# Kernel optimization log

Measured on AMD Instinct MI355X. Metric: run time of the kernel, lower is better.

## Reference

```python
import jax, jax.numpy as jnp
import numpy as np

N_NODES = 100000
N_EDGES = 1600000
F_IN = 128      # dataset.num_features
HID = 128       # hidden_dim (heads=1)
HID_POST = 128  # hidden_dim_post
EDGE_DIM = 16
N_CLASSES = 16
NEG_SLOPE = 0.2  # PyG GATConv default leaky_relu slope


def setup_inputs() -> dict:
    key = jax.random.key(0)
    ks = jax.random.split(key, 16)
    s = 0.1  # weight scale
    inp = {
        "x": jax.random.normal(ks[0], (N_NODES, F_IN), jnp.float32),
        "edge_attr": jax.random.normal(ks[1], (N_EDGES, EDGE_DIM), jnp.float32),
        "W0": jax.random.normal(ks[2], (F_IN, HID), jnp.float32) * s,
        "a_src0": jax.random.normal(ks[3], (HID,), jnp.float32) * s,
        "a_dst0": jax.random.normal(ks[4], (HID,), jnp.float32) * s,
        "We0": jax.random.normal(ks[5], (EDGE_DIM, HID), jnp.float32) * s,
        "a_e0": jax.random.normal(ks[6], (HID,), jnp.float32) * s,
        "b0": jnp.zeros((HID,), jnp.float32),
        "W1": jax.random.normal(ks[7], (HID, HID), jnp.float32) * s,
        "a_src1": jax.random.normal(ks[8], (HID,), jnp.float32) * s,
        "a_dst1": jax.random.normal(ks[9], (HID,), jnp.float32) * s,
        "We1": jax.random.normal(ks[10], (EDGE_DIM, HID), jnp.float32) * s,
        "a_e1": jax.random.normal(ks[11], (HID,), jnp.float32) * s,
        "b1": jnp.zeros((HID,), jnp.float32),
        "lin1_w": jax.random.normal(ks[12], (HID, HID_POST), jnp.float32) * s,
        "lin1_b": jnp.zeros((HID_POST,), jnp.float32),
        "lin2_w": jax.random.normal(ks[13], (HID_POST, N_CLASSES), jnp.float32) * s,
        "lin2_b": jnp.zeros((N_CLASSES,), jnp.float32),
        "edge_index": jax.random.randint(ks[14], (2, N_EDGES), 0, N_NODES, jnp.int64),
    }
    return inp


def gat_conv(x, src, dst, edge_attr, W, a_s, a_d, We, a_e, b):
    """PyG GATConv, heads=1, edge_dim set, add_self_loops=True (fill_value='mean')."""
    n = x.shape[0]
    xl = x @ W                       # [N, HID] shared lin for src/dst
    alpha_src_n = xl @ a_s           # [N]
    alpha_dst_n = xl @ a_d           # [N]
    # self loops: edge_attr filled with per-target-node mean of incoming edge_attr
    deg = jax.ops.segment_sum(jnp.ones(src.shape[0], x.dtype), dst, num_segments=n)
    ea_mean = jax.ops.segment_sum(edge_attr, dst, num_segments=n) / jnp.maximum(deg, 1.0)[:, None]
    loop = jnp.arange(n, dtype=src.dtype)
    src_f = jnp.concatenate([src, loop])
    dst_f = jnp.concatenate([dst, loop])
    ea_f = jnp.concatenate([edge_attr, ea_mean], axis=0)  # [E+N, EDGE_DIM]
    alpha_edge = (ea_f @ We) @ a_e                        # [E+N]
    alpha = jax.nn.leaky_relu(
        alpha_src_n[src_f] + alpha_dst_n[dst_f] + alpha_edge, NEG_SLOPE
    )
    # segment softmax over destination node (every node has its self loop -> nonempty)
    amax = jax.ops.segment_max(alpha, dst_f, num_segments=n)
    ex = jnp.exp(alpha - amax[dst_f])
    denom = jax.ops.segment_sum(ex, dst_f, num_segments=n)
    w = ex / denom[dst_f]                                 # [E+N]
    out = jax.ops.segment_sum(xl[src_f] * w[:, None], dst_f, num_segments=n)
    return out + b


def reference(x, edge_attr, W0, a_src0, a_dst0, We0, a_e0, b0,
              W1, a_src1, a_dst1, We1, a_e1, b1,
              lin1_w, lin1_b, lin2_w, lin2_b, edge_index):
    src, dst = edge_index[0], edge_index[1]
    # dropout layers are identity in eval mode
    h = jax.nn.relu(gat_conv(x, src, dst, edge_attr, W0, a_src0, a_dst0, We0, a_e0, b0))
    h = jax.nn.relu(gat_conv(h, src, dst, edge_attr, W1, a_src1, a_dst1, We1, a_e1, b1))
    h = jax.nn.relu(h @ lin1_w + lin1_b)
    logits = h @ lin2_w + lin2_b
    return jax.nn.log_softmax(logits, axis=-1)
```

## Files before the change

kernel.cpp:

```cpp
#include <hip/hip_runtime.h>
#include <math.h>

#define N_NODES 100000
#define N_EDGES 1600000
#define NEG 0.2f
#define MAXDEG 128
#define WPB 4

__device__ __forceinline__ float lrelu(float x){ return x > 0.f ? x : NEG*x; }
__device__ __forceinline__ unsigned short f2bf(float f){
  unsigned int u = __float_as_uint(f);
  u += 0x7FFFu + ((u >> 16) & 1u);
  return (unsigned short)(u >> 16);
}

__global__ __launch_bounds__(256) void k_deg(const int* __restrict__ dst, int* __restrict__ deg){
  int e = blockIdx.x*256 + threadIdx.x;
  if (e < N_EDGES) atomicAdd(&deg[dst[e]], 1);
}

__global__ __launch_bounds__(256) void k_scan_a(const int* __restrict__ deg, int* __restrict__ incl, int* __restrict__ bsum){
  __shared__ int s[256];
  int t = threadIdx.x; int i = blockIdx.x*256 + t;
  int v = (i < N_NODES) ? deg[i] : 0;
  s[t] = v; __syncthreads();
  for (int off=1; off<256; off<<=1){
    int u = (t>=off)? s[t-off] : 0; __syncthreads();
    s[t] += u; __syncthreads();
  }
  if (i < N_NODES) incl[i] = s[t];
  if (t == 255) bsum[blockIdx.x] = s[t];
}
__global__ __launch_bounds__(512) void k_scan_b(const int* __restrict__ bsum, int* __restrict__ bexcl, int nb,
    const float* __restrict__ We0, const float* __restrict__ ae0,
    const float* __restrict__ We1, const float* __restrict__ ae1, float* __restrict__ wea01){
  __shared__ int s[512];
  int t = threadIdx.x;
  int v = (t<nb)? bsum[t] : 0;
  s[t] = v; __syncthreads();
  for (int off=1; off<512; off<<=1){
    int u = (t>=off)? s[t-off] : 0; __syncthreads();
    s[t] += u; __syncthreads();
  }
  if (t<nb) bexcl[t] = s[t]-v;
  if (t < 16){
    float acc = 0.f;
    for (int j=0;j<128;j++) acc += We0[t*128+j]*ae0[j];
    wea01[t]=acc;
  } else if (t < 32){
    int r = t - 16;
    float acc = 0.f;
    for (int j=0;j<128;j++) acc += We1[r*128+j]*ae1[j];
    wea01[t]=acc;
  }
}
__global__ __launch_bounds__(256) void k_scan_c(const int* __restrict__ incl, const int* __restrict__ deg,
    const int* __restrict__ bexcl, int* __restrict__ rowptr){
  int i = blockIdx.x*256+threadIdx.x;
  if (i < N_NODES) rowptr[i] = incl[i] - deg[i] + bexcl[blockIdx.x];
  if (i == 0) rowptr[N_NODES] = N_EDGES;
}

__global__ __launch_bounds__(256) void k_fillf(const int* __restrict__ src, const int* __restrict__ dst,
     const int* __restrict__ rowptr, int* __restrict__ fill,
     const float* __restrict__ eatt, const float* __restrict__ wea01, uint4* __restrict__ csr){
  int e = blockIdx.x*256+threadIdx.x;
  if (e >= N_EDGES) return;
  const float4* w4 = (const float4*)wea01;
  float4 u0=w4[0], u1=w4[1], u2=w4[2], u3=w4[3];
  float4 v0=w4[4], v1=w4[5], v2=w4[6], v3=w4[7];
  const float4* p = (const float4*)(eatt + (size_t)e*16);
  float4 a0=p[0], a1=p[1], a2=p[2], a3=p[3];
  float ae0 = a0.x*u0.x+a0.y*u0.y+a0.z*u0.z+a0.w*u0.w
            + a1.x*u1.x+a1.y*u1.y+a1.z*u1.z+a1.w*u1.w
            + a2.x*u2.x+a2.y*u2.y+a2.z*u2.z+a2.w*u2.w
            + a3.x*u3.x+a3.y*u3.y+a3.z*u3.z+a3.w*u3.w;
  float ae1 = a0.x*v0.x+a0.y*v0.y+a0.z*v0.z+a0.w*v0.w
            + a1.x*v1.x+a1.y*v1.y+a1.z*v1.z+a1.w*v1.w
            + a2.x*v2.x+a2.y*v2.y+a2.z*v2.z+a2.w*v2.w
            + a3.x*v3.x+a3.y*v3.y+a3.z*v3.z+a3.w*v3.w;
  int d = dst[e];
  int pos = rowptr[d] + atomicAdd(&fill[d], 1);
  csr[pos] = make_uint4((unsigned)src[e], __float_as_uint(ae0), __float_as_uint(ae1), 0u);
}

__global__ __launch_bounds__(256) void k_gemm(const float* __restrict__ X, const float* __restrict__ W,
    const float* __restrict__ bias, float* __restrict__ Y, unsigned short* __restrict__ Ybf,
    const float* __restrict__ a_s, const float* __restrict__ a_d,
    float* __restrict__ asrc, float* __restrict__ adst, int M, int relu){
  __shared__ float Xs[16][68];
  __shared__ float Ws[16][128];
  __shared__ float as_s[128], ad_s[128];
  int t = threadIdx.x;
  if (a_s && t < 128){ as_s[t] = a_s[t]; ad_s[t] = a_d[t]; }
  int row0 = blockIdx.x * 64;
  int tc = t & 15, tr = t >> 4;
  int c0 = tc*8, r0 = tr*4;
  int lr = t >> 2, lc = (t & 3) << 2;
  int wk = t >> 4, wc = (t & 15) * 8;
  float acc[4][8];
  #pragma unroll
  for (int i=0;i<4;i++)
    #pragma unroll
    for (int j=0;j<8;j++) acc[i][j]=0.f;
  int gr = row0 + lr;
  for (int k0=0; k0<128; k0+=16){
    float4 xv = make_float4(0.f,0.f,0.f,0.f);
    if (gr < M) xv = *(const float4*)(X + (size_t)gr*128 + k0 + lc);
    float4 wv0 = *(const float4*)(W + (size_t)(k0+wk)*128 + wc);
    float4 wv1 = *(const float4*)(W + (size_t)(k0+wk)*128 + wc + 4);
    __syncthreads();
    Xs[lc+0][lr]=xv.x; Xs[lc+1][lr]=xv.y; Xs[lc+2][lr]=xv.z; Xs[lc+3][lr]=xv.w;
    *(float4*)&Ws[wk][wc]   = wv0;
    *(float4*)&Ws[wk][wc+4] = wv1;
    __syncthreads();
    #pragma unroll
    for (int kk=0;kk<16;kk++){
      float4 a  = *(const float4*)&Xs[kk][r0];
      float4 b0 = *(const float4*)&Ws[kk][c0];
      float4 b1 = *(const float4*)&Ws[kk][c0+4];
      float av[4] = {a.x,a.y,a.z,a.w};
      float bv[8] = {b0.x,b0.y,b0.z,b0.w,b1.x,b1.y,b1.z,b1.w};
      #pragma unroll
      for (int i=0;i<4;i++)
        #pragma unroll
        for (int j=0;j<8;j++) acc[i][j] += av[i]*bv[j];
    }
  }
  #pragma unroll
  for (int i=0;i<4;i++){
    int r = row0 + r0 + i;
    float v[8];
    #pragma unroll
    for (int j=0;j<8;j++){
      float u = acc[i][j] + (bias ? bias[c0+j] : 0.f);
      v[j] = relu ? fmaxf(u, 0.f) : u;
    }
    if (r < M){
      if (Y){
        *(float4*)(Y + (size_t)r*128 + c0)     = make_float4(v[0],v[1],v[2],v[3]);
        *(float4*)(Y + (size_t)r*128 + c0 + 4) = make_float4(v[4],v[5],v[6],v[7]);
      }
      if (Ybf){
        uint4 pk;
        pk.x = (unsigned)f2bf(v[0]) | ((unsigned)f2bf(v[1])<<16);
        pk.y = (unsigned)f2bf(v[2]) | ((unsigned)f2bf(v[3])<<16);
        pk.z = (unsigned)f2bf(v[4]) | ((unsigned)f2bf(v[5])<<16);
        pk.w = (unsigned)f2bf(v[6]) | ((unsigned)f2bf(v[7])<<16);
        *(uint4*)(Ybf + (size_t)r*128 + c0) = pk;
      }
    }
    if (a_s){
      float s=0.f, d=0.f;
      #pragma unroll
      for (int j=0;j<8;j++){ s += v[j]*as_s[c0+j]; d += v[j]*ad_s[c0+j]; }
      #pragma unroll
      for (int off=1; off<16; off<<=1){ s += __shfl_xor(s,off); d += __shfl_xor(d,off); }
      if ((t & 15)==0 && r < M){ asrc[r]=s; adst[r]=d; }
    }
  }
}

__global__ __launch_bounds__(256) void k_agg(const int* __restrict__ rowptr, const uint4* __restrict__ csr,
    const float* __restrict__ asrc, const float* __restrict__ adst,
    const unsigned short* __restrict__ xlbf,
    const float* __restrict__ bias, float* __restrict__ out, int relu, int layer){
  int w = threadIdx.x >> 6;
  int lane = threadIdx.x & 63;
  int n = blockIdx.x * WPB + w;
  __shared__ float wbuf[WPB][MAXDEG];
  __shared__ int   sbuf[WPB][MAXDEG];
  const unsigned int* xb = (const unsigned int*)xlbf;
  int s0 = rowptr[n], s1 = rowptr[n+1];
  int deg = s1 - s0;
  float adst_n = adst[n];
  float m_edge = -1e30f;
  float sae = 0.f;
  for (int base=0; base<deg; base+=64){
    int i = base + lane;
    float a = -1e30f;
    if (i < deg){
      uint4 p4 = csr[s0 + i];
      int sx = (int)p4.x;
      float ae = __uint_as_float(layer ? p4.z : p4.y);
      float av = lrelu(asrc[sx] + adst_n + ae);
      if (i < MAXDEG){ wbuf[w][i] = av; sbuf[w][i] = sx; }
      a = av;
      sae += ae;
    }
    for (int off=32; off; off>>=1) a = fmaxf(a, __shfl_xor(a, off));
    m_edge = fmaxf(m_edge, a);
  }
  for (int off=32; off; off>>=1) sae += __shfl_xor(sae, off);
  float aloop_n = sae / fmaxf((float)deg, 1.f);
  float al = lrelu(asrc[n] + adst_n + aloop_n);
  float m = fmaxf(m_edge, al);
  float p = 0.f;
  for (int i=lane; i<deg; i+=64){
    float av;
    if (i < MAXDEG) av = wbuf[w][i];
    else { uint4 p4 = csr[s0+i];
           av = lrelu(asrc[p4.x] + adst_n + __uint_as_float(layer ? p4.z : p4.y)); }
    float ev = __expf(av - m);
    if (i < MAXDEG) wbuf[w][i] = ev;
    p += ev;
  }
  for (int off=32; off; off>>=1) p += __shfl_xor(p, off);
  float wl = __expf(al - m);
  float denom = p + wl;
  __syncthreads();
  int g = lane >> 4, cl = lane & 15;
  float acc[8];
  #pragma unroll
  for (int j=0;j<8;j++) acc[j]=0.f;
  if (g == 0){
    uint4 v = *(const uint4*)(xb + (size_t)n*64 + cl*4);
    unsigned int uu[4] = {v.x,v.y,v.z,v.w};
    #pragma unroll
    for (int q=0;q<4;q++){
      acc[2*q]   += wl * __uint_as_float(uu[q] << 16);
      acc[2*q+1] += wl * __uint_as_float(uu[q] & 0xFFFF0000u);
    }
  }
  for (int i=0; i<deg; i+=4){
    int idx = i + g;
    int sx = n; float we = 0.f;
    if (idx < deg){
      if (idx < MAXDEG){ sx = sbuf[w][idx]; we = wbuf[w][idx]; }
      else {
        uint4 p4 = csr[s0+idx]; sx = (int)p4.x;
        we = __expf(lrelu(asrc[sx] + adst_n + __uint_as_float(layer ? p4.z : p4.y)) - m);
      }
    }
    uint4 v = *(const uint4*)(xb + (size_t)sx*64 + cl*4);
    unsigned int uu[4] = {v.x,v.y,v.z,v.w};
    #pragma unroll
    for (int q=0;q<4;q++){
      acc[2*q]   += we * __uint_as_float(uu[q] << 16);
      acc[2*q+1] += we * __uint_as_float(uu[q] & 0xFFFF0000u);
    }
  }
  #pragma unroll
  for (int j=0;j<8;j++){
    acc[j] += __shfl_xor(acc[j], 16);
    acc[j] += __shfl_xor(acc[j], 32);
  }
  if (lane < 16){
    float inv = 1.f/denom;
    float4 b0 = *(const float4*)(bias + cl*8);
    float4 b1 = *(const float4*)(bias + cl*8 + 4);
    float o[8];
    o[0]=acc[0]*inv+b0.x; o[1]=acc[1]*inv+b0.y; o[2]=acc[2]*inv+b0.z; o[3]=acc[3]*inv+b0.w;
    o[4]=acc[4]*inv+b1.x; o[5]=acc[5]*inv+b1.y; o[6]=acc[6]*inv+b1.z; o[7]=acc[7]*inv+b1.w;
    if (relu){
      #pragma unroll
      for (int j=0;j<8;j++) o[j]=fmaxf(o[j],0.f);
    }
    *(float4*)(out + (size_t)n*128 + cl*8)     = make_float4(o[0],o[1],o[2],o[3]);
    *(float4*)(out + (size_t)n*128 + cl*8 + 4) = make_float4(o[4],o[5],o[6],o[7]);
  }
}

__global__ __launch_bounds__(256) void k_mlp(const float* __restrict__ X, const float* __restrict__ W,
    const float* __restrict__ bias, const float* __restrict__ w2, const float* __restrict__ b2,
    float* __restrict__ out, int M){
  __shared__ float Xs[16][68];
  __shared__ float Ws[16][128];
  __shared__ float hs[64*132];
  __shared__ float b2s[16];
  int t = threadIdx.x;
  int row0 = blockIdx.x * 64;
  int tc = t & 15, tr = t >> 4;
  int c0 = tc*8, r0 = tr*4;
  int lr = t >> 2, lc = (t & 3) << 2;
  int wk = t >> 4, wc = (t & 15) * 8;
  float acc[4][8];
  #pragma unroll
  for (int i=0;i<4;i++)
    #pragma unroll
    for (int j=0;j<8;j++) acc[i][j]=0.f;
  int gr = row0 + lr;
  for (int k0=0; k0<128; k0+=16){
    float4 xv = make_float4(0.f,0.f,0.f,0.f);
    if (gr < M) xv = *(const float4*)(X + (size_t)gr*128 + k0 + lc);
    float4 wv0 = *(const float4*)(W + (size_t)(k0+wk)*128 + wc);
    float4 wv1 = *(const float4*)(W + (size_t)(k0+wk)*128 + wc + 4);
    __syncthreads();
    Xs[lc+0][lr]=xv.x; Xs[lc+1][lr]=xv.y; Xs[lc+2][lr]=xv.z; Xs[lc+3][lr]=xv.w;
    *(float4*)&Ws[wk][wc]   = wv0;
    *(float4*)&Ws[wk][wc+4] = wv1;
    __syncthreads();
    #pragma unroll
    for (int kk=0;kk<16;kk++){
      float4 a  = *(const float4*)&Xs[kk][r0];
      float4 b0 = *(const float4*)&Ws[kk][c0];
      float4 b1 = *(const float4*)&Ws[kk][c0+4];
      float av[4] = {a.x,a.y,a.z,a.w};
      float bv[8] = {b0.x,b0.y,b0.z,b0.w,b1.x,b1.y,b1.z,b1.w};
      #pragma unroll
      for (int i=0;i<4;i++)
        #pragma unroll
        for (int j=0;j<8;j++) acc[i][j] += av[i]*bv[j];
    }
  }
  __syncthreads();
  float* wflat = &Ws[0][0];
  #pragma unroll
  for (int i=0;i<2;i++) ((float4*)wflat)[t + i*256] = ((const float4*)w2)[t + i*256];
  if (t < 16) b2s[t] = b2[t];
  #pragma unroll
  for (int i=0;i<4;i++){
    float v[8];
    #pragma unroll
    for (int j=0;j<8;j++) v[j] = fmaxf(acc[i][j] + bias[c0+j], 0.f);
    int lrow = r0 + i;
    *(float4*)&hs[lrow*132 + c0]     = make_float4(v[0],v[1],v[2],v[3]);
    *(float4*)&hs[lrow*132 + c0 + 4] = make_float4(v[4],v[5],v[6],v[7]);
  }
  __syncthreads();
  int nl = t >> 2, cq = (t & 3) * 4;
  int n = row0 + nl;
  if (n < M){
    float a0=b2s[cq], a1=b2s[cq+1], a2=b2s[cq+2], a3=b2s[cq+3];
    const float* hp = &hs[nl*132];
    #pragma unroll 8
    for (int k=0;k<128;k++){
      float hv = hp[k];
      float4 w4 = *(const float4*)&wflat[k*16 + cq];
      a0 += hv*w4.x; a1 += hv*w4.y; a2 += hv*w4.z; a3 += hv*w4.w;
    }
    float m = fmaxf(fmaxf(a0,a1), fmaxf(a2,a3));
    m = fmaxf(m, __shfl_xor(m, 1));
    m = fmaxf(m, __shfl_xor(m, 2));
    float s = __expf(a0-m)+__expf(a1-m)+__expf(a2-m)+__expf(a3-m);
    s += __shfl_xor(s, 1);
    s += __shfl_xor(s, 2);
    float lse = m + __logf(s);
    *(float4*)(out + (size_t)n*16 + cq) = make_float4(a0-lse, a1-lse, a2-lse, a3-lse);
  }
}

extern "C" void kernel_launch(void* const* d_in, const int* in_sizes, int n_in,
                              void* d_out, int out_size, void* d_ws, size_t ws_size,
                              hipStream_t stream){
  const float* x    = (const float*)d_in[0];
  const float* eatt = (const float*)d_in[1];
  const float* W0   = (const float*)d_in[2];
  const float* as0  = (const float*)d_in[3];
  const float* ad0  = (const float*)d_in[4];
  const float* We0  = (const float*)d_in[5];
  const float* ae0  = (const float*)d_in[6];
  const float* b0   = (const float*)d_in[7];
  const float* W1   = (const float*)d_in[8];
  const float* as1  = (const float*)d_in[9];
  const float* ad1  = (const float*)d_in[10];
  const float* We1  = (const float*)d_in[11];
  const float* ae1  = (const float*)d_in[12];
  const float* b1   = (const float*)d_in[13];
  const float* l1w  = (const float*)d_in[14];
  const float* l1b  = (const float*)d_in[15];
  const float* l2w  = (const float*)d_in[16];
  const float* l2b  = (const float*)d_in[17];
  const int*   ei   = (const int*)d_in[18];
  const int* srcI = ei;
  const int* dstI = ei + N_EDGES;
  float* out = (float*)d_out;

  char* p = (char*)d_ws;
  auto alloc = [&](size_t bytes)->char*{ char* r = p; p += (bytes + 255) & ~255ull; return r; };
  unsigned short* Abf = (unsigned short*)alloc((size_t)N_NODES*128*2);
  float* B       = (float*)alloc((size_t)N_NODES*128*4);
  float* asrc    = (float*)alloc((size_t)N_NODES*4);
  float* adst    = (float*)alloc((size_t)N_NODES*4);
  float* wea01   = (float*)alloc(128);
  int* deg     = (int*)alloc((size_t)N_NODES*4);
  int* fill    = (int*)alloc((size_t)N_NODES*4);
  int* rowptr  = (int*)alloc((size_t)(N_NODES+1)*4);
  uint4* csr   = (uint4*)alloc((size_t)N_EDGES*16);
  int* incl    = (int*)alloc((size_t)N_NODES*4);
  int* bsum    = (int*)alloc(512*4);
  int* bexcl   = (int*)alloc(512*4);

  const int NB_E = (N_EDGES+255)/256;
  const int NB_N = (N_NODES+255)/256;
  const int NB_W = N_NODES/WPB;
  const int NB_G = (N_NODES+63)/64;

  hipMemsetAsync(deg,  0, (size_t)N_NODES*4, stream);
  hipMemsetAsync(fill, 0, (size_t)N_NODES*4, stream);
  k_deg   <<<NB_E,256,0,stream>>>(dstI, deg);
  k_scan_a<<<NB_N,256,0,stream>>>(deg, incl, bsum);
  k_scan_b<<<1,  512,0,stream>>>(bsum, bexcl, NB_N, We0, ae0, We1, ae1, wea01);
  k_scan_c<<<NB_N,256,0,stream>>>(incl, deg, bexcl, rowptr);
  k_fillf <<<NB_E,256,0,stream>>>(srcI, dstI, rowptr, fill, eatt, wea01, csr);

  k_gemm <<<NB_G,256,0,stream>>>(x, W0, nullptr, nullptr, Abf, as0, ad0, asrc, adst, N_NODES, 0);
  k_agg  <<<NB_W,256,0,stream>>>(rowptr, csr, asrc, adst, Abf, b0, B, 1, 0);

  k_gemm <<<NB_G,256,0,stream>>>(B, W1, nullptr, nullptr, Abf, as1, ad1, asrc, adst, N_NODES, 0);
  k_agg  <<<NB_W,256,0,stream>>>(rowptr, csr, asrc, adst, Abf, b1, B, 1, 1);

  k_mlp  <<<NB_G,256,0,stream>>>(B, l1w, l1b, l2w, l2b, out, N_NODES);
}
```

Measured before the change: 683.7 us.

## Record per-edge rank in degree pass and precompute edge attention scalars there

The degree-counting kernel now keeps the return value of its atomic increment as each edge's rank within its destination row. It also computes the two per-edge attention scalars from edge_attr, with every block recomputing the We·a_e projection into shared memory. The fill kernel then places each edge at rowptr+rank without a second round of atomics and without rereading edge_attr. The fill array and its memset go away, and the rank and scalar scratch buffers reuse the Abf and B workspaces. In exchange, every block of the degree kernel repeats the 32×128 weight dot products, and the extra rank and scalar arrays are written and read back.

```diff
diff --git a/kernel.cpp b/kernel.cpp
--- a/kernel.cpp
+++ b/kernel.cpp
@@ -14,9 +14,36 @@
   return (unsigned short)(u >> 16);
 }
 
-__global__ __launch_bounds__(256) void k_deg(const int* __restrict__ dst, int* __restrict__ deg){
-  int e = blockIdx.x*256 + threadIdx.x;
-  if (e < N_EDGES) atomicAdd(&deg[dst[e]], 1);
+__global__ __launch_bounds__(256) void k_deg(const int* __restrict__ dst, const float* __restrict__ eatt,
+    const float* __restrict__ We0, const float* __restrict__ ae0,
+    const float* __restrict__ We1, const float* __restrict__ ae1,
+    int* __restrict__ deg, int* __restrict__ rank, float2* __restrict__ ae01){
+  __shared__ float wea[32];
+  int t = threadIdx.x;
+  if (t < 32){
+    const float* W = (t < 16) ? We0 : We1;
+    const float* a = (t < 16) ? ae0 : ae1;
+    int r = t & 15;
+    float acc = 0.f;
+    #pragma unroll
+    for (int j=0;j<128;j++) acc += W[r*128+j]*a[j];
+    wea[t] = acc;
+  }
+  __syncthreads();
+  int e = blockIdx.x*256 + t;
+  if (e >= N_EDGES) return;
+  const float4* p = (const float4*)(eatt + (size_t)e*16);
+  float4 a0=p[0], a1=p[1], a2=p[2], a3=p[3];
+  float f0 = a0.x*wea[0] +a0.y*wea[1] +a0.z*wea[2] +a0.w*wea[3]
+           + a1.x*wea[4] +a1.y*wea[5] +a1.z*wea[6] +a1.w*wea[7]
+           + a2.x*wea[8] +a2.y*wea[9] +a2.z*wea[10]+a2.w*wea[11]
+           + a3.x*wea[12]+a3.y*wea[13]+a3.z*wea[14]+a3.w*wea[15];
+  float f1 = a0.x*wea[16]+a0.y*wea[17]+a0.z*wea[18]+a0.w*wea[19]
+           + a1.x*wea[20]+a1.y*wea[21]+a1.z*wea[22]+a1.w*wea[23]
+           + a2.x*wea[24]+a2.y*wea[25]+a2.z*wea[26]+a2.w*wea[27]
+           + a3.x*wea[28]+a3.y*wea[29]+a3.z*wea[30]+a3.w*wea[31];
+  rank[e] = atomicAdd(&deg[dst[e]], 1);
+  ae01[e] = make_float2(f0, f1);
 }
 
 __global__ __launch_bounds__(256) void k_scan_a(const int* __restrict__ deg, int* __restrict__ incl, int* __restrict__ bsum){
@@ -31,9 +58,7 @@
   if (i < N_NODES) incl[i] = s[t];
   if (t == 255) bsum[blockIdx.x] = s[t];
 }
-__global__ __launch_bounds__(512) void k_scan_b(const int* __restrict__ bsum, int* __restrict__ bexcl, int nb,
-    const float* __restrict__ We0, const float* __restrict__ ae0,
-    const float* __restrict__ We1, const float* __restrict__ ae1, float* __restrict__ wea01){
+__global__ __launch_bounds__(512) void k_scan_b(const int* __restrict__ bsum, int* __restrict__ bexcl, int nb){
   __shared__ int s[512];
   int t = threadIdx.x;
   int v = (t<nb)? bsum[t] : 0;
@@ -43,16 +68,6 @@
     s[t] += u; __syncthreads();
   }
   if (t<nb) bexcl[t] = s[t]-v;
-  if (t < 16){
-    float acc = 0.f;
-    for (int j=0;j<128;j++) acc += We0[t*128+j]*ae0[j];
-    wea01[t]=acc;
-  } else if (t < 32){
-    int r = t - 16;
-    float acc = 0.f;
-    for (int j=0;j<128;j++) acc += We1[r*128+j]*ae1[j];
-    wea01[t]=acc;
-  }
 }
 __global__ __launch_bounds__(256) void k_scan_c(const int* __restrict__ incl, const int* __restrict__ deg,
     const int* __restrict__ bexcl, int* __restrict__ rowptr){
@@ -62,26 +77,14 @@
 }
 
 __global__ __launch_bounds__(256) void k_fillf(const int* __restrict__ src, const int* __restrict__ dst,
-     const int* __restrict__ rowptr, int* __restrict__ fill,
-     const float* __restrict__ eatt, const float* __restrict__ wea01, uint4* __restrict__ csr){
+     const int* __restrict__ rank, const float2* __restrict__ ae01,
+     const int* __restrict__ rowptr, uint4* __restrict__ csr){
   int e = blockIdx.x*256+threadIdx.x;
   if (e >= N_EDGES) return;
-  const float4* w4 = (const float4*)wea01;
-  float4 u0=w4[0], u1=w4[1], u2=w4[2], u3=w4[3];
-  float4 v0=w4[4], v1=w4[5], v2=w4[6], v3=w4[7];
-  const float4* p = (const float4*)(eatt + (size_t)e*16);
-  float4 a0=p[0], a1=p[1], a2=p[2], a3=p[3];
-  float ae0 = a0.x*u0.x+a0.y*u0.y+a0.z*u0.z+a0.w*u0.w
-            + a1.x*u1.x+a1.y*u1.y+a1.z*u1.z+a1.w*u1.w
-            + a2.x*u2.x+a2.y*u2.y+a2.z*u2.z+a2.w*u2.w
-            + a3.x*u3.x+a3.y*u3.y+a3.z*u3.z+a3.w*u3.w;
-  float ae1 = a0.x*v0.x+a0.y*v0.y+a0.z*v0.z+a0.w*v0.w
-            + a1.x*v1.x+a1.y*v1.y+a1.z*v1.z+a1.w*v1.w
-            + a2.x*v2.x+a2.y*v2.y+a2.z*v2.z+a2.w*v2.w
-            + a3.x*v3.x+a3.y*v3.y+a3.z*v3.z+a3.w*v3.w;
   int d = dst[e];
-  int pos = rowptr[d] + atomicAdd(&fill[d], 1);
-  csr[pos] = make_uint4((unsigned)src[e], __float_as_uint(ae0), __float_as_uint(ae1), 0u);
+  float2 ae = ae01[e];
+  int pos = rowptr[d] + rank[e];
+  csr[pos] = make_uint4((unsigned)src[e], __float_as_uint(ae.x), __float_as_uint(ae.y), 0u);
 }
 
 __global__ __launch_bounds__(256) void k_gemm(const float* __restrict__ X, const float* __restrict__ W,
@@ -229,7 +232,7 @@
       if (idx < MAXDEG){ sx = sbuf[w][idx]; we = wbuf[w][idx]; }
       else {
         uint4 p4 = csr[s0+idx]; sx = (int)p4.x;
-        we = __expf(lrelu(asrc[sx] + adst_n + __uint_as_float(layer ? p4.z : p4.y)) - m);
+        we = __expf(lrelu(asrc[p4.x] + adst_n + __uint_as_float(layer ? p4.z : p4.y)) - m);
       }
     }
     uint4 v = *(const uint4*)(xb + (size_t)sx*64 + cl*4);
@@ -372,14 +375,14 @@
   float* B       = (float*)alloc((size_t)N_NODES*128*4);
   float* asrc    = (float*)alloc((size_t)N_NODES*4);
   float* adst    = (float*)alloc((size_t)N_NODES*4);
-  float* wea01   = (float*)alloc(128);
   int* deg     = (int*)alloc((size_t)N_NODES*4);
-  int* fill    = (int*)alloc((size_t)N_NODES*4);
   int* rowptr  = (int*)alloc((size_t)(N_NODES+1)*4);
   uint4* csr   = (uint4*)alloc((size_t)N_EDGES*16);
   int* incl    = (int*)alloc((size_t)N_NODES*4);
   int* bsum    = (int*)alloc(512*4);
   int* bexcl   = (int*)alloc(512*4);
+  float2* ae01 = (float2*)Abf;
+  int*    rank = (int*)B;
 
   const int NB_E = (N_EDGES+255)/256;
   const int NB_N = (N_NODES+255)/256;
@@ -387,12 +390,11 @@
   const int NB_G = (N_NODES+63)/64;
 
   hipMemsetAsync(deg,  0, (size_t)N_NODES*4, stream);
-  hipMemsetAsync(fill, 0, (size_t)N_NODES*4, stream);
-  k_deg   <<<NB_E,256,0,stream>>>(dstI, deg);
+  k_deg   <<<NB_E,256,0,stream>>>(dstI, eatt, We0, ae0, We1, ae1, deg, rank, ae01);
   k_scan_a<<<NB_N,256,0,stream>>>(deg, incl, bsum);
-  k_scan_b<<<1,  512,0,stream>>>(bsum, bexcl, NB_N, We0, ae0, We1, ae1, wea01);
+  k_scan_b<<<1,  512,0,stream>>>(bsum, bexcl, NB_N);
   k_scan_c<<<NB_N,256,0,stream>>>(incl, deg, bexcl, rowptr);
-  k_fillf <<<NB_E,256,0,stream>>>(srcI, dstI, rowptr, fill, eatt, wea01, csr);
+  k_fillf <<<NB_E,256,0,stream>>>(srcI, dstI, rank, ae01, rowptr, csr);
 
   k_gemm <<<NB_G,256,0,stream>>>(x, W0, nullptr, nullptr, Abf, as0, ad0, asrc, adst, N_NODES, 0);
   k_agg  <<<NB_W,256,0,stream>>>(rowptr, csr, asrc, adst, Abf, b0, B, 1, 0);
```

After: 637.1 us. -6.8%, faster.
